# Kernel optimization log

Hardware: AMD Instinct MI355X
Metric: run time of the kernel (lower is better)

Reference implementation:

```python
import jax, jax.numpy as jnp
import numpy as np

IN_F = 4096
OUT_F = 4096
BATCH = 8192


def setup_inputs() -> dict:
    key = jax.random.key(0)
    ks = jax.random.split(key, 7)
    # Xavier-normal-ish mu, rho = -3 as in reset_parameters (plus small noise for generality)
    xav = float(np.sqrt(2.0 / (IN_F + OUT_F)))
    return {
        "x": jax.random.normal(ks[0], (BATCH, IN_F), jnp.float32),
        "weight_mu": jax.random.normal(ks[1], (OUT_F, IN_F), jnp.float32) * xav,
        "weight_rho": jnp.full((OUT_F, IN_F), -3.0, jnp.float32)
        + 0.1 * jax.random.normal(ks[2], (OUT_F, IN_F), jnp.float32),
        "bias_mu": jnp.zeros((OUT_F,), jnp.float32),
        "bias_rho": jnp.full((OUT_F,), -3.0, jnp.float32)
        + 0.1 * jax.random.normal(ks[3], (OUT_F,), jnp.float32),
        "weight_eps": jax.random.normal(ks[4], (OUT_F, IN_F), jnp.float32),
        "bias_eps": jax.random.normal(ks[5], (OUT_F,), jnp.float32),
    }


def reference(x, weight_mu, weight_rho, bias_mu, bias_rho, weight_eps, bias_eps):
    # sigma = log1p(exp(rho)) = softplus(rho); sampled weight = mu + sigma * eps
    weight = weight_mu + jax.nn.softplus(weight_rho) * weight_eps  # [out, in]
    bias = bias_mu + jax.nn.softplus(bias_rho) * bias_eps          # [out]
    # F.linear: x @ weight.T + bias
    return jnp.einsum("bi,oi->bo", x, weight) + bias
```

## Files before the change

### kernel.cpp

```cpp
#include <hip/hip_runtime.h>
#include <hip/hip_bf16.h>
#include <math.h>

typedef __bf16 bf16;
typedef __attribute__((ext_vector_type(8))) __bf16 bf16x8;
typedef __attribute__((ext_vector_type(4))) float f32x4;

typedef const uint32_t __attribute__((address_space(1)))* gp1_t;
typedef uint32_t __attribute__((address_space(3)))* lp3_t;

__device__ __forceinline__ void async_load16(const void* g, void* l) {
    __builtin_amdgcn_global_load_lds((gp1_t)g, (lp3_t)l, 16, 0, 0);
}

__device__ __forceinline__ float softplus_f(float x) {
    return fmaxf(x, 0.0f) + __logf(1.0f + __expf(-fabsf(x)));
}

#define IN_F  4096
#define OUT_F 4096
#define BATCH 8192

#define BM 256
#define BN 256

#define NXB ((BATCH * IN_F) / (256 * 8))
#define NWB ((OUT_F * IN_F) / (256 * 8))

__global__ __launch_bounds__(256) void prologue(
    const float* __restrict__ x,
    const float* __restrict__ mu, const float* __restrict__ rho,
    const float* __restrict__ eps,
    bf16* __restrict__ xb, bf16* __restrict__ W)
{
    const int b = blockIdx.x;
    if (b < NXB) {
        const int i = (b * 256 + threadIdx.x) * 8;
        float4 a = *(const float4*)(x + i);
        float4 c = *(const float4*)(x + i + 4);
        bf16x8 o;
        o[0] = (bf16)a.x; o[1] = (bf16)a.y; o[2] = (bf16)a.z; o[3] = (bf16)a.w;
        o[4] = (bf16)c.x; o[5] = (bf16)c.y; o[6] = (bf16)c.z; o[7] = (bf16)c.w;
        *(bf16x8*)(xb + i) = o;
    } else {
        const int i = ((b - NXB) * 256 + threadIdx.x) * 8;
        bf16x8 w;
#pragma unroll
        for (int h = 0; h < 2; ++h) {
            float4 m = *(const float4*)(mu + i + h * 4);
            float4 r = *(const float4*)(rho + i + h * 4);
            float4 e = *(const float4*)(eps + i + h * 4);
            w[h * 4 + 0] = (bf16)(m.x + softplus_f(r.x) * e.x);
            w[h * 4 + 1] = (bf16)(m.y + softplus_f(r.y) * e.y);
            w[h * 4 + 2] = (bf16)(m.z + softplus_f(r.z) * e.z);
            w[h * 4 + 3] = (bf16)(m.w + softplus_f(r.w) * e.w);
        }
        *(bf16x8*)(W + i) = w;
    }
}

__global__ __launch_bounds__(512, 2) void gemm_bt_bias(
    const bf16* __restrict__ A,
    const bf16* __restrict__ W,
    const float* __restrict__ bmu, const float* __restrict__ brho,
    const float* __restrict__ beps,
    float* __restrict__ C)
{
    __shared__ __align__(16) bf16 lds[2][2][2][128 * 64];

    const int tid  = threadIdx.x;
    const int lane = tid & 63;
    const int l15  = lane & 15;
    const int quad = lane >> 4;

    const int bn = blockIdx.x & 15;
    const int bm = blockIdx.x >> 4;
    const int row0 = bm * BM;
    const int col0 = bn * BN;

    const int wave = tid >> 6;
    const int wmh = wave >> 2;
    const int wnq = wave & 3;
    const int wbh = wnq >> 1;
    const int nb  = (wnq & 1) * 64;

    const f32x4 zero = {0.f, 0.f, 0.f, 0.f};
    f32x4 acc[8][4];
#pragma unroll
    for (int i2 = 0; i2 < 8; ++i2)
#pragma unroll
        for (int j2 = 0; j2 < 4; ++j2) acc[i2][j2] = zero;

    const int ldsw = (tid & ~63) * 16;

    auto STAGE = [&](int m, int t) {
        const int buf = t & 1;
        const int k0  = (t < (IN_F / 64) ? t : (IN_F / 64 - 1)) << 6;
        const bf16* g = (m < 2) ? A : W;
        const int gr  = ((m < 2) ? row0 : col0) + ((m & 1) << 7);
        char* slot = (char*)&lds[buf][m >> 1][m & 1][0];
#pragma unroll
        for (int j = 0; j < 2; ++j) {
            const int p    = j * 8192 + tid * 16;
            const int r    = p >> 7;
            const int irow = (p & 127) ^ ((r & 7) << 4);
            async_load16(g + (size_t)(gr + r) * IN_F + k0 + (irow >> 1),
                         slot + j * 8192 + ldsw);
        }
    };

#define FRAG(SLOT, ROW, KQ)                                                  \
    (*(const bf16x8*)((SLOT) + (ROW) * 128 +                                 \
                      (((KQ) * 64 + quad * 16) ^ (((ROW) & 7) << 4))))

#define MFMA_Q(AF, BF, MB, NB_)                                              \
    {                                                                        \
        _Pragma("unroll")                                                    \
        for (int kq = 0; kq < 2; ++kq)                                       \
            _Pragma("unroll")                                                \
            for (int f = 0; f < 4; ++f)                                      \
                _Pragma("unroll")                                            \
                for (int g2 = 0; g2 < 2; ++g2)                               \
                    acc[(MB) + f][(NB_) + g2] =                              \
                        __builtin_amdgcn_mfma_f32_16x16x32_bf16(             \
                            AF[f][kq], BF[g2][kq],                           \
                            acc[(MB) + f][(NB_) + g2], 0, 0, 0);             \
    }

    STAGE(0, 0); STAGE(1, 0); STAGE(2, 0); STAGE(3, 0);
    STAGE(0, 1); STAGE(1, 1);
    asm volatile("s_waitcnt vmcnt(4)" ::: "memory");
    asm volatile("s_barrier" ::: "memory");

    bf16x8 a0[4][2], a1[4][2], b0[2][2], b1[2][2];

    for (int i = 0; i < IN_F / 128; ++i) {
#pragma unroll
        for (int h = 0; h < 2; ++h) {
            const int tc = 2 * i + h;
            const char* SA = (const char*)&lds[h][0][wmh][0];
            const char* SB = (const char*)&lds[h][1][wbh][0];

#pragma unroll
            for (int f = 0; f < 4; ++f) {
                a0[f][0] = FRAG(SA, f * 16 + l15, 0);
                a0[f][1] = FRAG(SA, f * 16 + l15, 1);
            }
#pragma unroll
            for (int f = 0; f < 2; ++f) {
                b0[f][0] = FRAG(SB, nb + f * 16 + l15, 0);
                b0[f][1] = FRAG(SB, nb + f * 16 + l15, 1);
            }
            STAGE(2, tc + 1);
            asm volatile("s_barrier" ::: "memory");
            asm volatile("s_waitcnt lgkmcnt(0)" ::: "memory");
            __builtin_amdgcn_sched_barrier(0);
            __builtin_amdgcn_s_setprio(1);
            MFMA_Q(a0, b0, 0, 0);
            __builtin_amdgcn_s_setprio(0);
            asm volatile("s_barrier" ::: "memory");

#pragma unroll
            for (int f = 0; f < 4; ++f) {
                a1[f][0] = FRAG(SA, 64 + f * 16 + l15, 0);
                a1[f][1] = FRAG(SA, 64 + f * 16 + l15, 1);
            }
#pragma unroll
            for (int f = 0; f < 2; ++f) {
                b1[f][0] = FRAG(SB, nb + 32 + f * 16 + l15, 0);
                b1[f][1] = FRAG(SB, nb + 32 + f * 16 + l15, 1);
            }
            STAGE(3, tc + 1);
            asm volatile("s_barrier" ::: "memory");
            asm volatile("s_waitcnt lgkmcnt(0)" ::: "memory");
            __builtin_amdgcn_sched_barrier(0);
            __builtin_amdgcn_s_setprio(1);
            MFMA_Q(a0, b1, 0, 2);
            __builtin_amdgcn_s_setprio(0);
            asm volatile("s_barrier" ::: "memory");

            STAGE(0, tc + 2);
            asm volatile("s_barrier" ::: "memory");
            __builtin_amdgcn_s_setprio(1);
            MFMA_Q(a1, b0, 4, 0);
            __builtin_amdgcn_s_setprio(0);
            asm volatile("s_barrier" ::: "memory");

            STAGE(1, tc + 2);
            asm volatile("s_barrier" ::: "memory");
            __builtin_amdgcn_s_setprio(1);
            MFMA_Q(a1, b1, 4, 2);
            __builtin_amdgcn_s_setprio(0);
            asm volatile("s_waitcnt vmcnt(4)" ::: "memory");
            asm volatile("s_barrier" ::: "memory");
        }
    }

    float bias[4];
#pragma unroll
    for (int f = 0; f < 4; ++f) {
        const int col = col0 + wnq * 64 + f * 16 + l15;
        bias[f] = bmu[col] + softplus_f(brho[col]) * beps[col];
    }

#pragma unroll
    for (int mf = 0; mf < 8; ++mf) {
#pragma unroll
        for (int r = 0; r < 4; ++r) {
            const size_t row = (size_t)row0 + wmh * 128 + mf * 16 + quad * 4 + r;
#pragma unroll
            for (int f = 0; f < 4; ++f) {
                const int col = col0 + wnq * 64 + f * 16 + l15;
                C[row * OUT_F + col] = acc[mf][f][r] + bias[f];
            }
        }
    }
#undef FRAG
#undef MFMA_Q
}

extern "C" void kernel_launch(void* const* d_in, const int* in_sizes, int n_in,
                              void* d_out, int out_size, void* d_ws, size_t ws_size,
                              hipStream_t stream) {
    const float* x    = (const float*)d_in[0];
    const float* wmu  = (const float*)d_in[1];
    const float* wrho = (const float*)d_in[2];
    const float* bmu  = (const float*)d_in[3];
    const float* brho = (const float*)d_in[4];
    const float* weps = (const float*)d_in[5];
    const float* beps = (const float*)d_in[6];
    float* out = (float*)d_out;

    bf16* xb = (bf16*)d_ws;
    bf16* W  = (bf16*)((char*)d_ws + (size_t)BATCH * IN_F * sizeof(bf16));

    prologue<<<NXB + NWB, 256, 0, stream>>>(x, wmu, wrho, weps, xb, W);

    gemm_bt_bias<<<(BATCH / BM) * (OUT_F / BN), 512, 0, stream>>>(
        xb, W, bmu, brho, beps, out);
}
```

Baseline: 663.0 us.

## Restructure GEMM main loop to prefetch LDS fragments across phases and use grid-stride prologue

The GEMM inner loop is reordered so B fragments for both halves are read up front and the next tile's A fragments are prefetched from the other LDS buffer during the current MFMA phase. Partial lgkmcnt waits replace full drains, and the MFMA quadrant order changes, with fewer barriers per phase. The goal is to hide LDS read latency behind MFMA work and cut synchronisation stalls. The prologue also becomes a fixed-size grid-stride loop to reduce block launch overhead. The partial waits and the cross-buffer prefetch raise the risk of race or ordering bugs.

```diff
diff --git a/kernel.cpp b/kernel.cpp
--- a/kernel.cpp
+++ b/kernel.cpp
@@ -23,9 +23,7 @@
 
 #define BM 256
 #define BN 256
-
-#define NXB ((BATCH * IN_F) / (256 * 8))
-#define NWB ((OUT_F * IN_F) / (256 * 8))
+#define PGRID 2048
 
 __global__ __launch_bounds__(256) void prologue(
     const float* __restrict__ x,
@@ -33,17 +31,20 @@
     const float* __restrict__ eps,
     bf16* __restrict__ xb, bf16* __restrict__ W)
 {
-    const int b = blockIdx.x;
-    if (b < NXB) {
-        const int i = (b * 256 + threadIdx.x) * 8;
+    const int stride = PGRID * 256;
+    const int nx = BATCH * IN_F / 8;
+    const int nw = OUT_F * IN_F / 8;
+    for (int u = blockIdx.x * 256 + threadIdx.x; u < nx; u += stride) {
+        const int i = u * 8;
         float4 a = *(const float4*)(x + i);
         float4 c = *(const float4*)(x + i + 4);
         bf16x8 o;
         o[0] = (bf16)a.x; o[1] = (bf16)a.y; o[2] = (bf16)a.z; o[3] = (bf16)a.w;
         o[4] = (bf16)c.x; o[5] = (bf16)c.y; o[6] = (bf16)c.z; o[7] = (bf16)c.w;
         *(bf16x8*)(xb + i) = o;
-    } else {
-        const int i = ((b - NXB) * 256 + threadIdx.x) * 8;
+    }
+    for (int u = blockIdx.x * 256 + threadIdx.x; u < nw; u += stride) {
+        const int i = u * 8;
         bf16x8 w;
 #pragma unroll
         for (int h = 0; h < 2; ++h) {
@@ -127,72 +128,82 @@
                             acc[(MB) + f][(NB_) + g2], 0, 0, 0);             \
     }
 
-    STAGE(0, 0); STAGE(1, 0); STAGE(2, 0); STAGE(3, 0);
-    STAGE(0, 1); STAGE(1, 1);
-    asm volatile("s_waitcnt vmcnt(4)" ::: "memory");
+    bf16x8 a0[4][2], a1[4][2], b0[2][2], b1[2][2];
+
+    STAGE(0, 0); STAGE(1, 0); STAGE(2, 0);
+    STAGE(3, 0); STAGE(0, 1); STAGE(1, 1);
+    asm volatile("s_waitcnt vmcnt(6)" ::: "memory");
     asm volatile("s_barrier" ::: "memory");
-
-    bf16x8 a0[4][2], a1[4][2], b0[2][2], b1[2][2];
+    {
+        const char* SA = (const char*)&lds[0][0][wmh][0];
+#pragma unroll
+        for (int f = 0; f < 4; ++f) {
+            a0[f][0] = FRAG(SA, f * 16 + l15, 0);
+            a0[f][1] = FRAG(SA, f * 16 + l15, 1);
+        }
+    }
 
     for (int i = 0; i < IN_F / 128; ++i) {
 #pragma unroll
         for (int h = 0; h < 2; ++h) {
             const int tc = 2 * i + h;
-            const char* SA = (const char*)&lds[h][0][wmh][0];
-            const char* SB = (const char*)&lds[h][1][wbh][0];
-
-#pragma unroll
-            for (int f = 0; f < 4; ++f) {
-                a0[f][0] = FRAG(SA, f * 16 + l15, 0);
-                a0[f][1] = FRAG(SA, f * 16 + l15, 1);
-            }
+            const char* SA  = (const char*)&lds[h][0][wmh][0];
+            const char* SB  = (const char*)&lds[h][1][wbh][0];
+            const char* SA1 = (const char*)&lds[h ^ 1][0][wmh][0];
+
+            asm volatile("s_waitcnt vmcnt(4)" ::: "memory");
+            asm volatile("s_barrier" ::: "memory");
 #pragma unroll
             for (int f = 0; f < 2; ++f) {
                 b0[f][0] = FRAG(SB, nb + f * 16 + l15, 0);
                 b0[f][1] = FRAG(SB, nb + f * 16 + l15, 1);
             }
+#pragma unroll
+            for (int f = 0; f < 2; ++f) {
+                b1[f][0] = FRAG(SB, nb + 32 + f * 16 + l15, 0);
+                b1[f][1] = FRAG(SB, nb + 32 + f * 16 + l15, 1);
+            }
             STAGE(2, tc + 1);
-            asm volatile("s_barrier" ::: "memory");
-            asm volatile("s_waitcnt lgkmcnt(0)" ::: "memory");
+            asm volatile("s_waitcnt lgkmcnt(4)" ::: "memory");
             __builtin_amdgcn_sched_barrier(0);
             __builtin_amdgcn_s_setprio(1);
             MFMA_Q(a0, b0, 0, 0);
             __builtin_amdgcn_s_setprio(0);
-            asm volatile("s_barrier" ::: "memory");
-
+
+            asm volatile("s_waitcnt vmcnt(4)" ::: "memory");
+            asm volatile("s_barrier" ::: "memory");
 #pragma unroll
             for (int f = 0; f < 4; ++f) {
                 a1[f][0] = FRAG(SA, 64 + f * 16 + l15, 0);
                 a1[f][1] = FRAG(SA, 64 + f * 16 + l15, 1);
             }
-#pragma unroll
-            for (int f = 0; f < 2; ++f) {
-                b1[f][0] = FRAG(SB, nb + 32 + f * 16 + l15, 0);
-                b1[f][1] = FRAG(SB, nb + 32 + f * 16 + l15, 1);
-            }
             STAGE(3, tc + 1);
-            asm volatile("s_barrier" ::: "memory");
-            asm volatile("s_waitcnt lgkmcnt(0)" ::: "memory");
+            asm volatile("s_waitcnt lgkmcnt(8)" ::: "memory");
             __builtin_amdgcn_sched_barrier(0);
             __builtin_amdgcn_s_setprio(1);
             MFMA_Q(a0, b1, 0, 2);
             __builtin_amdgcn_s_setprio(0);
-            asm volatile("s_barrier" ::: "memory");
-
+
+            asm volatile("s_waitcnt vmcnt(4)" ::: "memory");
+            asm volatile("s_barrier" ::: "memory");
+#pragma unroll
+            for (int f = 0; f < 4; ++f) {
+                a0[f][0] = FRAG(SA1, f * 16 + l15, 0);
+                a0[f][1] = FRAG(SA1, f * 16 + l15, 1);
+            }
             STAGE(0, tc + 2);
-            asm volatile("s_barrier" ::: "memory");
+            asm volatile("s_waitcnt lgkmcnt(8)" ::: "memory");
+            __builtin_amdgcn_sched_barrier(0);
+            __builtin_amdgcn_s_setprio(1);
+            MFMA_Q(a1, b1, 4, 2);
+            __builtin_amdgcn_s_setprio(0);
+
+            asm volatile("s_waitcnt vmcnt(4)" ::: "memory");
+            asm volatile("s_barrier" ::: "memory");
+            STAGE(1, tc + 2);
             __builtin_amdgcn_s_setprio(1);
             MFMA_Q(a1, b0, 4, 0);
             __builtin_amdgcn_s_setprio(0);
-            asm volatile("s_barrier" ::: "memory");
-
-            STAGE(1, tc + 2);
-            asm volatile("s_barrier" ::: "memory");
-            __builtin_amdgcn_s_setprio(1);
-            MFMA_Q(a1, b1, 4, 2);
-            __builtin_amdgcn_s_setprio(0);
-            asm volatile("s_waitcnt vmcnt(4)" ::: "memory");
-            asm volatile("s_barrier" ::: "memory");
         }
     }
 
@@ -234,7 +245,7 @@
     bf16* xb = (bf16*)d_ws;
     bf16* W  = (bf16*)((char*)d_ws + (size_t)BATCH * IN_F * sizeof(bf16));
 
-    prologue<<<NXB + NWB, 256, 0, stream>>>(x, wmu, wrho, weps, xb, W);
+    prologue<<<PGRID, 256, 0, stream>>>(x, wmu, wrho, weps, xb, W);
 
     gemm_bt_bias<<<(BATCH / BM) * (OUT_F / BN), 512, 0, stream>>>(
         xb, W, bmu, brho, beps, out);
```

Result: slower. 775.8 us (+17.0%).
